# Performance work log

Hardware: AMD Instinct MI355X
Metric: run time of the kernel (lower is better)

## Reference

```python
import jax, jax.numpy as jnp
from jax import lax
import numpy as np

B = 4096          # batch
EMBED = 32        # embed_dim
HEADS = 2
MEM_SIZE = 4096
MEM_DIM = 256
TOPK = 10
LN_EPS = 1e-5


def setup_inputs() -> dict:
    key = jax.random.key(0)
    ks = jax.random.split(key, 32)
    rn = lambda i, shape, s=0.05: (jax.random.normal(ks[i], shape) * s).astype(jnp.float32)
    return {
        'x': jax.random.normal(ks[0], (B, 1, 28, 28), dtype=jnp.float32),
        'patch_w': rn(1, (32, 1, 4, 4)), 'patch_b': rn(2, (32,)),
        'blk_ln1_g': jnp.ones((2, 32), jnp.float32), 'blk_ln1_b': jnp.zeros((2, 32), jnp.float32),
        'blk_inproj_w': rn(3, (2, 96, 32)), 'blk_inproj_b': rn(4, (2, 96)),
        'blk_outproj_w': rn(5, (2, 32, 32)), 'blk_outproj_b': rn(6, (2, 32)),
        'blk_ln2_g': jnp.ones((2, 32), jnp.float32), 'blk_ln2_b': jnp.zeros((2, 32), jnp.float32),
        'blk_ff1_w': rn(7, (2, 128, 32)), 'blk_ff1_b': rn(8, (2, 128)),
        'blk_ff2_w': rn(9, (2, 32, 128)), 'blk_ff2_b': rn(10, (2, 32)),
        'lat_w': rn(11, (256, 1568)), 'lat_b': rn(12, (256,)),
        'memory': jax.random.normal(ks[13], (MEM_SIZE, MEM_DIM), dtype=jnp.float32),
        'dec_w': rn(14, (3136, 256)), 'dec_b': rn(15, (3136,)),
        'upt1_w': rn(16, (64, 32, 4, 4)), 'upt1_b': rn(17, (32,)),
        'c1_w': rn(18, (32, 32, 3, 3)), 'c1_b': rn(19, (32,)),
        'upt2_w': rn(20, (32, 16, 4, 4)), 'upt2_b': rn(21, (16,)),
        'c2_w': rn(22, (8, 16, 3, 3)), 'c2_b': rn(23, (8,)),
        'c3_w': rn(24, (1, 8, 1, 1)), 'c3_b': rn(25, (1,)),
    }


def _ln(x, g, b):
    m = jnp.mean(x, -1, keepdims=True)
    v = jnp.mean((x - m) ** 2, -1, keepdims=True)
    return (x - m) / jnp.sqrt(v + LN_EPS) * g + b


def _conv2d(x, w, b, stride=1, pad=0):
    out = lax.conv_general_dilated(x, w, (stride, stride), ((pad, pad), (pad, pad)),
                                   dimension_numbers=('NCHW', 'OIHW', 'NCHW'))
    return out + b[None, :, None, None]


def _conv_transpose2d(x, w, b, stride, pad):
    # w in torch layout [in, out, kh, kw]; equivalent fractionally-strided conv
    w_f = jnp.flip(w, (2, 3)).transpose(1, 0, 2, 3)  # OIHW
    k = w.shape[2]
    p = k - 1 - pad
    out = lax.conv_general_dilated(x, w_f, (1, 1), ((p, p), (p, p)),
                                   lhs_dilation=(stride, stride),
                                   dimension_numbers=('NCHW', 'OIHW', 'NCHW'))
    return out + b[None, :, None, None]


def _mha(x, wi, bi, wo, bo):
    Bn, S, D = x.shape
    Dh = D // HEADS
    qkv = x @ wi.T + bi                                  # [B,S,3D]
    q, k, v = jnp.split(qkv, 3, axis=-1)
    sp = lambda t: t.reshape(Bn, S, HEADS, Dh).transpose(0, 2, 1, 3)
    q, k, v = sp(q), sp(k), sp(v)
    scores = jnp.einsum('bhqd,bhkd->bhqk', q, k) / jnp.sqrt(jnp.asarray(Dh, x.dtype))
    att = jax.nn.softmax(scores, axis=-1)
    o = jnp.einsum('bhqk,bhkd->bhqd', att, v).transpose(0, 2, 1, 3).reshape(Bn, S, D)
    return o @ wo.T + bo


def _memory_read(latent, memory):
    # cosine-sim topk softmax-weighted gather (F.normalize eps=1e-12)
    mn = memory / jnp.clip(jnp.linalg.norm(memory, axis=1, keepdims=True), 1e-12)
    xn = latent / jnp.clip(jnp.linalg.norm(latent, axis=1, keepdims=True), 1e-12)
    sim = xn @ mn.T                                       # [B, MEM_SIZE]
    topk_sim, topk_idx = lax.top_k(sim, TOPK)
    w = jax.nn.softmax(topk_sim, axis=1)                  # [B, TOPK]
    sel = memory[topk_idx]                                # [B, TOPK, MEM_DIM]
    return jnp.einsum('bk,bkd->bd', w, sel)


def _forward(x, patch_w, patch_b, blk_ln1_g, blk_ln1_b, blk_inproj_w, blk_inproj_b,
             blk_outproj_w, blk_outproj_b, blk_ln2_g, blk_ln2_b, blk_ff1_w, blk_ff1_b,
             blk_ff2_w, blk_ff2_b, lat_w, lat_b, memory, dec_w, dec_b,
             upt1_w, upt1_b, c1_w, c1_b, upt2_w, upt2_b, c2_w, c2_b, c3_w, c3_b):
    Bn = x.shape[0]
    h = _conv2d(x, patch_w, patch_b, stride=4)            # [B,32,7,7]
    t = h.reshape(Bn, EMBED, 49).transpose(0, 2, 1)       # [B,49,32]
    for i in range(2):                                    # two SwinBlocks
        t = t + _mha(_ln(t, blk_ln1_g[i], blk_ln1_b[i]),
                     blk_inproj_w[i], blk_inproj_b[i], blk_outproj_w[i], blk_outproj_b[i])
        f = _ln(t, blk_ln2_g[i], blk_ln2_b[i])
        f = jax.nn.gelu(f @ blk_ff1_w[i].T + blk_ff1_b[i], approximate=False)
        t = t + (f @ blk_ff2_w[i].T + blk_ff2_b[i])
    latent = t.reshape(Bn, -1) @ lat_w.T + lat_b          # [B,256]
    mem_latent = _memory_read(latent, memory)             # [B,256]
    d = (mem_latent @ dec_w.T + dec_b).reshape(Bn, 64, 7, 7)  # dropout=eval identity
    d = jax.nn.relu(_conv_transpose2d(d, upt1_w, upt1_b, 2, 1))   # [B,32,14,14]
    d = jax.nn.relu(_conv2d(d, c1_w, c1_b, 1, 1))
    d = jax.nn.relu(_conv_transpose2d(d, upt2_w, upt2_b, 2, 1))   # [B,16,28,28]
    d = jax.nn.relu(_conv2d(d, c2_w, c2_b, 1, 1))                 # [B,8,28,28]
    return _conv2d(d, c3_w, c3_b, 1, 0)                           # [B,1,28,28]


def reference(x, patch_w, patch_b, blk_ln1_g, blk_ln1_b, blk_inproj_w, blk_inproj_b,
              blk_outproj_w, blk_outproj_b, blk_ln2_g, blk_ln2_b, blk_ff1_w, blk_ff1_b,
              blk_ff2_w, blk_ff2_b, lat_w, lat_b, memory, dec_w, dec_b,
              upt1_w, upt1_b, c1_w, c1_b, upt2_w, upt2_b, c2_w, c2_b, c3_w, c3_b):
    return _forward(x, patch_w, patch_b, blk_ln1_g, blk_ln1_b, blk_inproj_w, blk_inproj_b,
                    blk_outproj_w, blk_outproj_b, blk_ln2_g, blk_ln2_b, blk_ff1_w, blk_ff1_b,
                    blk_ff2_w, blk_ff2_b, lat_w, lat_b, memory, dec_w, dec_b,
                    upt1_w, upt1_b, c1_w, c1_b, upt2_w, upt2_b, c2_w, c2_b, c3_w, c3_b)
```

## Files before the change

### kernel.cpp

```cpp
#include <hip/hip_runtime.h>
#include <math.h>

#define B_TOT 4096
#define CHUNK 4096

typedef _Float16 half_t;
typedef _Float16 h2 __attribute__((ext_vector_type(2)));
typedef _Float16 h8v __attribute__((ext_vector_type(8)));
typedef float f4v __attribute__((ext_vector_type(4)));
typedef float f2v __attribute__((ext_vector_type(2)));

#if __has_builtin(__builtin_amdgcn_fdot2)
#define FDOT2(a, b, c) __builtin_amdgcn_fdot2((a), (b), (c), false)
#else
#define FDOT2(a, b, c) fmaf((float)(a)[1], (float)(b)[1], fmaf((float)(a)[0], (float)(b)[0], (c)))
#endif

#define KSTR 36
#define VSTR 34
#define KBYTES (49 * 72)
#define WAVE_LDS (49 * 72 + 49 * 136)
#define WI_OFF  (4 * WAVE_LDS)
#define BLOCK_LDS (WI_OFF + 12288)

__global__ __launch_bounds__(256) void k_tokens(
    const float* __restrict__ x, const float* __restrict__ pw, const float* __restrict__ pb,
    const float* __restrict__ ln1g, const float* __restrict__ ln1b,
    const float* __restrict__ wi, const float* __restrict__ bi,
    const float* __restrict__ wo, const float* __restrict__ bo,
    const float* __restrict__ ln2g, const float* __restrict__ ln2b,
    const float* __restrict__ w1, const float* __restrict__ fb1,
    const float* __restrict__ w2t, const float* __restrict__ fb2,
    float* __restrict__ tokens)
{
    __shared__ __align__(16) unsigned char Lraw[BLOCK_LDS];
    const int tid = threadIdx.x;
    const int wv = tid >> 6, lane = tid & 63;
    const int b = blockIdx.x * 4 + wv;
    half_t* Kb = (half_t*)(Lraw + wv * WAVE_LDS);
    float*  Vb = (float*)(Lraw + wv * WAVE_LDS + KBYTES);
    const float* wiL = (const float*)(Lraw + WI_OFF);
    float* Lf = (float*)Lraw;
    const bool is_tok = lane < 49;
    const int s = is_tok ? lane : 48;
    const int py = s / 7, px = s % 7;

    {
        const float4* srcw = (const float4*)(wi);
        float4* dstw = (float4*)(Lraw + WI_OFF);
        for (int e = tid; e < 768; e += 256) dstw[e] = srcw[e];
    }

    f2v xv2[8];
    const float* xb = x + (size_t)b * 784 + py * 112 + px * 4;
    #pragma unroll
    for (int r = 0; r < 4; ++r) {
        float4 vq = *(const float4*)(xb + r * 28);
        f2v lo; lo[0] = vq.x; lo[1] = vq.y;
        f2v hi; hi[0] = vq.z; hi[1] = vq.w;
        xv2[2 * r] = lo; xv2[2 * r + 1] = hi;
    }
    f2v t2[16];
    #pragma unroll
    for (int c = 0; c < 32; ++c) {
        const float* wr = pw + c * 16;
        f2v a2 = (f2v){0.f, 0.f};
        #pragma unroll
        for (int c2 = 0; c2 < 4; ++c2) {
            float4 wq = *(const float4*)&wr[4 * c2];
            f2v w0; w0[0] = wq.x; w0[1] = wq.y;
            f2v w1v; w1v[0] = wq.z; w1v[1] = wq.w;
            a2 += xv2[2 * c2] * w0;
            a2 += xv2[2 * c2 + 1] * w1v;
        }
        t2[c >> 1][c & 1] = pb[c] + a2[0] + a2[1];
    }

    for (int blk = 0; blk < 2; ++blk) {
        const float* bib = bi + blk * 96;

        f2v mu2 = (f2v){0.f, 0.f};
        #pragma unroll
        for (int i = 0; i < 16; ++i) mu2 += t2[i];
        float mu = (mu2[0] + mu2[1]) * 0.03125f;
        f2v mub; mub[0] = mu; mub[1] = mu;
        f2v var2 = (f2v){0.f, 0.f};
        #pragma unroll
        for (int i = 0; i < 16; ++i) { f2v d = t2[i] - mub; var2 += d * d; }
        float rstd = rsqrtf((var2[0] + var2[1]) * 0.03125f + 1e-5f);
        f2v rstd2; rstd2[0] = rstd; rstd2[1] = rstd;
        f2v xn2[16];
        {
            const f2v* g2 = (const f2v*)(ln1g + blk * 32);
            const f2v* bl2 = (const f2v*)(ln1b + blk * 32);
            #pragma unroll
            for (int i = 0; i < 16; ++i)
                xn2[i] = (t2[i] - mub) * rstd2 * g2[i] + bl2[i];
        }

        __syncthreads();

        #pragma unroll 4
        for (int d = 0; d < 32; ++d) {
            const float* wr = wiL + (32 + d) * 32;
            f2v a2 = (f2v){0.f, 0.f};
            #pragma unroll
            for (int c2 = 0; c2 < 8; ++c2) {
                float4 wq = *(const float4*)&wr[4 * c2];
                f2v w0; w0[0] = wq.x; w0[1] = wq.y;
                f2v w1v; w1v[0] = wq.z; w1v[1] = wq.w;
                a2 += xn2[2 * c2] * w0;
                a2 += xn2[2 * c2 + 1] * w1v;
            }
            if (is_tok) Kb[s * KSTR + d] = (half_t)(bib[32 + d] + a2[0] + a2[1]);
        }
        #pragma unroll 4
        for (int d = 0; d < 32; ++d) {
            const float* wr = wiL + (64 + d) * 32;
            f2v a2 = (f2v){0.f, 0.f};
            #pragma unroll
            for (int c2 = 0; c2 < 8; ++c2) {
                float4 wq = *(const float4*)&wr[4 * c2];
                f2v w0; w0[0] = wq.x; w0[1] = wq.y;
                f2v w1v; w1v[0] = wq.z; w1v[1] = wq.w;
                a2 += xn2[2 * c2] * w0;
                a2 += xn2[2 * c2 + 1] * w1v;
            }
            if (is_tok) Vb[s * VSTR + d] = bib[64 + d] + a2[0] + a2[1];
        }
        float q0[32];
        #pragma unroll 4
        for (int d = 0; d < 32; ++d) {
            const float* wr = wiL + d * 32;
            f2v a2 = (f2v){0.f, 0.f};
            #pragma unroll
            for (int c2 = 0; c2 < 8; ++c2) {
                float4 wq = *(const float4*)&wr[4 * c2];
                f2v w0; w0[0] = wq.x; w0[1] = wq.y;
                f2v w1v; w1v[0] = wq.z; w1v[1] = wq.w;
                a2 += xn2[2 * c2] * w0;
                a2 += xn2[2 * c2 + 1] * w1v;
            }
            q0[d] = (bib[d] + a2[0] + a2[1]) * 0.25f;
        }
        h2 qh[16];
        #pragma unroll
        for (int i = 0; i < 16; ++i) {
            h2 hh; hh[0] = (half_t)q0[2 * i]; hh[1] = (half_t)q0[2 * i + 1];
            qh[i] = hh;
        }

        __asm__ volatile("s_waitcnt lgkmcnt(0)" ::: "memory");

        f2v o2[16];
        #pragma unroll
        for (int i = 0; i < 16; ++i) o2[i] = (f2v){0.f, 0.f};
        float l0 = 0.f, l1 = 0.f;
        union H4 { double qd; h2 p[2]; };
        for (int j = 0; j < 49; ++j) {
            const double* kr = (const double*)(Kb + j * KSTR);
            const float* vr = Vb + j * VSTR;
            H4 u0, u1, u2, u3, w0, w1h, w2h, w3;
            u0.qd = kr[0]; u1.qd = kr[1]; u2.qd = kr[2]; u3.qd = kr[3];
            w0.qd = kr[4]; w1h.qd = kr[5]; w2h.qd = kr[6]; w3.qd = kr[7];
            float s0a = 0.f, s0b = 0.f, s1a = 0.f, s1b = 0.f;
            s0a = FDOT2(u0.p[0], qh[0], s0a); s0a = FDOT2(u0.p[1], qh[1], s0a);
            s0b = FDOT2(u1.p[0], qh[2], s0b); s0b = FDOT2(u1.p[1], qh[3], s0b);
            s0a = FDOT2(u2.p[0], qh[4], s0a); s0a = FDOT2(u2.p[1], qh[5], s0a);
            s0b = FDOT2(u3.p[0], qh[6], s0b); s0b = FDOT2(u3.p[1], qh[7], s0b);
            s1a = FDOT2(w0.p[0], qh[8], s1a); s1a = FDOT2(w0.p[1], qh[9], s1a);
            s1b = FDOT2(w1h.p[0], qh[10], s1b); s1b = FDOT2(w1h.p[1], qh[11], s1b);
            s1a = FDOT2(w2h.p[0], qh[12], s1a); s1a = FDOT2(w2h.p[1], qh[13], s1a);
            s1b = FDOT2(w3.p[0], qh[14], s1b); s1b = FDOT2(w3.p[1], qh[15], s1b);
            float p0 = __expf(s0a + s0b), p1 = __expf(s1a + s1b);
            l0 += p0; l1 += p1;
            f2v p02; p02[0] = p0; p02[1] = p0;
            f2v p12; p12[0] = p1; p12[1] = p1;
            #pragma unroll
            for (int i = 0; i < 8; ++i) {
                f2v va = *(const f2v*)&vr[2 * i];
                o2[i] += p02 * va;
                f2v vc = *(const f2v*)&vr[16 + 2 * i];
                o2[8 + i] += p12 * vc;
            }
        }
        {
            float il0 = 1.f / l0, il1 = 1.f / l1;
            f2v il02; il02[0] = il0; il02[1] = il0;
            f2v il12; il12[0] = il1; il12[1] = il1;
            #pragma unroll
            for (int i = 0; i < 8; ++i) { o2[i] *= il02; o2[8 + i] *= il12; }
        }

        #pragma unroll
        for (int c = 0; c < 32; ++c) {
            const float* wr = wo + blk * 1024 + c * 32;
            f2v a2 = (f2v){0.f, 0.f};
            #pragma unroll
            for (int c2 = 0; c2 < 8; ++c2) {
                float4 wq = *(const float4*)&wr[4 * c2];
                f2v w0; w0[0] = wq.x; w0[1] = wq.y;
                f2v w1v; w1v[0] = wq.z; w1v[1] = wq.w;
                a2 += o2[2 * c2] * w0;
                a2 += o2[2 * c2 + 1] * w1v;
            }
            t2[c >> 1][c & 1] += bo[blk * 32 + c] + a2[0] + a2[1];
        }

        mu2 = (f2v){0.f, 0.f};
        #pragma unroll
        for (int i = 0; i < 16; ++i) mu2 += t2[i];
        mu = (mu2[0] + mu2[1]) * 0.03125f;
        mub[0] = mu; mub[1] = mu;
        var2 = (f2v){0.f, 0.f};
        #pragma unroll
        for (int i = 0; i < 16; ++i) { f2v d = t2[i] - mub; var2 += d * d; }
        rstd = rsqrtf((var2[0] + var2[1]) * 0.03125f + 1e-5f);
        rstd2[0] = rstd; rstd2[1] = rstd;
        {
            const f2v* g2 = (const f2v*)(ln2g + blk * 32);
            const f2v* bl2 = (const f2v*)(ln2b + blk * 32);
            #pragma unroll
            for (int i = 0; i < 16; ++i)
                xn2[i] = (t2[i] - mub) * rstd2 * g2[i] + bl2[i];
        }

        __syncthreads();

        {
            const float4* src1 = (const float4*)(w1 + blk * 4096);
            const float4* src2 = (const float4*)(w2t + blk * 4096);
            float4* dst = (float4*)Lraw;
            for (int e = tid; e < 1024; e += 256) dst[e] = src1[e];
            for (int e = tid; e < 1024; e += 256) dst[1024 + e] = src2[e];
            if (blk == 0) {
                const float4* srcw = (const float4*)(wi + 3072);
                float4* dstw = (float4*)(Lraw + WI_OFF);
                for (int e = tid; e < 768; e += 256) dstw[e] = srcw[e];
            }
        }
        __syncthreads();

        const float* w2L = Lf + 4096;
        #pragma unroll 2
        for (int j = 0; j < 128; ++j) {
            const float* wr = Lf + j * 32;
            f2v h2a = (f2v){0.f, 0.f};
            #pragma unroll
            for (int c2 = 0; c2 < 8; ++c2) {
                float4 wq = *(const float4*)&wr[4 * c2];
                f2v w0; w0[0] = wq.x; w0[1] = wq.y;
                f2v w1v; w1v[0] = wq.z; w1v[1] = wq.w;
                h2a += xn2[2 * c2] * w0;
                h2a += xn2[2 * c2 + 1] * w1v;
            }
            float h = fb1[blk * 128 + j] + h2a[0] + h2a[1];
            h = 0.5f * h * (1.f + erff(h * 0.7071067811865476f));
            f2v hh; hh[0] = h; hh[1] = h;
            const float* w2r = w2L + j * 32;
            #pragma unroll
            for (int c2 = 0; c2 < 8; ++c2) {
                float4 wq = *(const float4*)&w2r[4 * c2];
                f2v w0; w0[0] = wq.x; w0[1] = wq.y;
                f2v w1v; w1v[0] = wq.z; w1v[1] = wq.w;
                t2[2 * c2]     += hh * w0;
                t2[2 * c2 + 1] += hh * w1v;
            }
        }
        {
            const f2v* fb22 = (const f2v*)(fb2 + blk * 32);
            #pragma unroll
            for (int i = 0; i < 16; ++i) t2[i] += fb22[i];
        }
    }

    if (is_tok) {
        float* op = tokens + (size_t)b * 1568 + s * 32;
        #pragma unroll
        for (int i = 0; i < 8; ++i) {
            float4 vv = make_float4(t2[2 * i][0], t2[2 * i][1],
                                    t2[2 * i + 1][0], t2[2 * i + 1][1]);
            *(float4*)&op[4 * i] = vv;
        }
    }
}

__global__ __launch_bounds__(256) void k_split(
    const float* __restrict__ lat_w, const float* __restrict__ memory,
    half_t* __restrict__ lwh, half_t* __restrict__ lwl,
    half_t* __restrict__ memh, half_t* __restrict__ meml,
    float* __restrict__ inv_norm)
{
    __shared__ float red[256];
    const int tid = threadIdx.x;
    size_t i = (size_t)blockIdx.x * 256 + tid;
    if (i < 401408) {
        float v = lat_w[i];
        half_t h = (half_t)v;
        lwh[i] = h; lwl[i] = (half_t)((v - (float)h) * 2048.0f);
    }
    float v = 0.f;
    if (i < 1048576) {
        v = memory[i];
        half_t h = (half_t)v;
        memh[i] = h; meml[i] = (half_t)((v - (float)h) * 2048.0f);
    }
    if (blockIdx.x < 4096) {
        red[tid] = v * v;
        __syncthreads();
        for (int s = 128; s > 0; s >>= 1) {
            if (tid < s) red[tid] += red[tid + s];
            __syncthreads();
        }
        if (tid == 0) inv_norm[blockIdx.x] = 1.f / fmaxf(sqrtf(red[0]), 1e-12f);
    }
}

__global__ __launch_bounds__(256) void k_sgemm(
    const float* __restrict__ A, const half_t* __restrict__ Bhg,
    const half_t* __restrict__ Blg, const float* __restrict__ bias,
    float* __restrict__ C, int M, int N, int K)
{
    __shared__ __align__(16) half_t Ah[64 * 40];
    __shared__ __align__(16) half_t Al[64 * 40];
    __shared__ __align__(16) half_t Bh[128 * 40];
    __shared__ __align__(16) half_t Bl[128 * 40];
    const int tid = threadIdx.x;
    const int n0 = blockIdx.x * 128, m0 = blockIdx.y * 64;
    const int w = tid >> 6, lane = tid & 63;
    const int wm = (w >> 1) * 32, wn = (w & 1) * 64;
    const int lr = lane & 15, lk = lane >> 4;

    const int ar = tid >> 2, aseg = (tid & 3) * 8;
    const int br = tid >> 1, bseg = (tid & 1) * 16;

    f4v acch[2][4], accm[2][4];
    #pragma unroll
    for (int i = 0; i < 2; ++i)
        #pragma unroll
        for (int j = 0; j < 4; ++j) {
            acch[i][j] = (f4v){0.f, 0.f, 0.f, 0.f};
            accm[i][j] = (f4v){0.f, 0.f, 0.f, 0.f};
        }

    for (int k0 = 0; k0 < K; k0 += 32) {
        {
            const float* ap = A + (size_t)(m0 + ar) * K + k0 + aseg;
            float4 a0 = *(const float4*)ap;
            float4 a1 = *(const float4*)(ap + 4);
            float av[8] = {a0.x, a0.y, a0.z, a0.w, a1.x, a1.y, a1.z, a1.w};
            h8v ah, al;
            #pragma unroll
            for (int i = 0; i < 8; ++i) {
                half_t h = (half_t)av[i];
                ah[i] = h;
                al[i] = (half_t)((av[i] - (float)h) * 2048.0f);
            }
            *(h8v*)&Ah[ar * 40 + aseg] = ah;
            *(h8v*)&Al[ar * 40 + aseg] = al;

            const half_t* bph = Bhg + (size_t)(n0 + br) * K + k0 + bseg;
            const half_t* bpl = Blg + (size_t)(n0 + br) * K + k0 + bseg;
            h8v bh0 = *(const h8v*)bph;
            h8v bh1 = *(const h8v*)(bph + 8);
            h8v bl0 = *(const h8v*)bpl;
            h8v bl1 = *(const h8v*)(bpl + 8);
            *(h8v*)&Bh[br * 40 + bseg]     = bh0;
            *(h8v*)&Bh[br * 40 + bseg + 8] = bh1;
            *(h8v*)&Bl[br * 40 + bseg]     = bl0;
            *(h8v*)&Bl[br * 40 + bseg + 8] = bl1;
        }
        __syncthreads();
        h8v afh[2], afl[2], bfh[4], bfl[4];
        #pragma unroll
        for (int i = 0; i < 2; ++i) {
            afh[i] = *(const h8v*)&Ah[(wm + i * 16 + lr) * 40 + lk * 8];
            afl[i] = *(const h8v*)&Al[(wm + i * 16 + lr) * 40 + lk * 8];
        }
        #pragma unroll
        for (int j = 0; j < 4; ++j) {
            bfh[j] = *(const h8v*)&Bh[(wn + j * 16 + lr) * 40 + lk * 8];
            bfl[j] = *(const h8v*)&Bl[(wn + j * 16 + lr) * 40 + lk * 8];
        }
        #pragma unroll
        for (int i = 0; i < 2; ++i)
            #pragma unroll
            for (int j = 0; j < 4; ++j) {
                acch[i][j] = __builtin_amdgcn_mfma_f32_16x16x32_f16(afh[i], bfh[j], acch[i][j], 0, 0, 0);
                accm[i][j] = __builtin_amdgcn_mfma_f32_16x16x32_f16(afh[i], bfl[j], accm[i][j], 0, 0, 0);
                accm[i][j] = __builtin_amdgcn_mfma_f32_16x16x32_f16(afl[i], bfh[j], accm[i][j], 0, 0, 0);
            }
        __syncthreads();
    }

    #pragma unroll
    for (int j = 0; j < 4; ++j) {
        int n = n0 + wn + j * 16 + lr;
        float bv = bias ? bias[n] : 0.f;
        #pragma unroll
        for (int i = 0; i < 2; ++i) {
            #pragma unroll
            for (int r = 0; r < 4; ++r) {
                int m = m0 + wm + i * 16 + lk * 4 + r;
                C[(size_t)m * N + n] = acch[i][j][r] + accm[i][j][r] * (1.0f / 2048.0f) + bv;
            }
        }
    }
}

__global__ __launch_bounds__(256) void k_dgemm(
    const float* __restrict__ A, const float* __restrict__ Bm,
    const float* __restrict__ bias, half_t* __restrict__ C,
    int M, int N, int K)
{
    __shared__ __align__(16) half_t As[64 * 40];
    __shared__ __align__(16) half_t Bs[128 * 40];
    const int tid = threadIdx.x;
    const int n0 = blockIdx.x * 128, m0 = blockIdx.y * 64;
    const int w = tid >> 6, lane = tid & 63;
    const int wm = (w >> 1) * 32, wn = (w & 1) * 64;
    const int lr = lane & 15, lk = lane >> 4;

    const int ar = tid >> 2, aseg = (tid & 3) * 8;
    const int br = tid >> 1, bseg = (tid & 1) * 16;

    f4v acc[2][4];
    #pragma unroll
    for (int i = 0; i < 2; ++i)
        #pragma unroll
        for (int j = 0; j < 4; ++j) acc[i][j] = (f4v){0.f, 0.f, 0.f, 0.f};

    for (int k0 = 0; k0 < K; k0 += 32) {
        {
            const float* ap = A + (size_t)(m0 + ar) * K + k0 + aseg;
            float4 a0 = *(const float4*)ap;
            float4 a1 = *(const float4*)(ap + 4);
            h8v ha;
            ha[0] = (half_t)a0.x; ha[1] = (half_t)a0.y;
            ha[2] = (half_t)a0.z; ha[3] = (half_t)a0.w;
            ha[4] = (half_t)a1.x; ha[5] = (half_t)a1.y;
            ha[6] = (half_t)a1.z; ha[7] = (half_t)a1.w;
            *(h8v*)&As[ar * 40 + aseg] = ha;

            const float* bp = Bm + (size_t)(n0 + br) * K + k0 + bseg;
            float4 b0 = *(const float4*)bp;
            float4 b1 = *(const float4*)(bp + 4);
            float4 b2 = *(const float4*)(bp + 8);
            float4 b3 = *(const float4*)(bp + 12);
            h8v hb0, hb1;
            hb0[0] = (half_t)b0.x; hb0[1] = (half_t)b0.y;
            hb0[2] = (half_t)b0.z; hb0[3] = (half_t)b0.w;
            hb0[4] = (half_t)b1.x; hb0[5] = (half_t)b1.y;
            hb0[6] = (half_t)b1.z; hb0[7] = (half_t)b1.w;
            hb1[0] = (half_t)b2.x; hb1[1] = (half_t)b2.y;
            hb1[2] = (half_t)b2.z; hb1[3] = (half_t)b2.w;
            hb1[4] = (half_t)b3.x; hb1[5] = (half_t)b3.y;
            hb1[6] = (half_t)b3.z; hb1[7] = (half_t)b3.w;
            *(h8v*)&Bs[br * 40 + bseg] = hb0;
            *(h8v*)&Bs[br * 40 + bseg + 8] = hb1;
        }
        __syncthreads();
        h8v af[2], bfr[4];
        #pragma unroll
        for (int i = 0; i < 2; ++i)
            af[i] = *(const h8v*)&As[(wm + i * 16 + lr) * 40 + lk * 8];
        #pragma unroll
        for (int j = 0; j < 4; ++j)
            bfr[j] = *(const h8v*)&Bs[(wn + j * 16 + lr) * 40 + lk * 8];
        #pragma unroll
        for (int i = 0; i < 2; ++i)
            #pragma unroll
            for (int j = 0; j < 4; ++j)
                acc[i][j] = __builtin_amdgcn_mfma_f32_16x16x32_f16(af[i], bfr[j], acc[i][j], 0, 0, 0);
        __syncthreads();
    }

    #pragma unroll
    for (int j = 0; j < 4; ++j) {
        int n = n0 + wn + j * 16 + lr;
        float bv = bias[n];
        #pragma unroll
        for (int i = 0; i < 2; ++i) {
            #pragma unroll
            for (int r = 0; r < 4; ++r) {
                int m = m0 + wm + i * 16 + lk * 4 + r;
                C[(size_t)m * N + n] = (half_t)fmaxf(acc[i][j][r] + bv, 0.f);
            }
        }
    }
}

__global__ __launch_bounds__(256) void k_fuse(
    const float* __restrict__ wt1, const float* __restrict__ upt1_b,
    const float* __restrict__ dec_w, const float* __restrict__ dec_b,
    float* __restrict__ Wf, float* __restrict__ bf)
{
    __shared__ float WL[4][64][32];
    const int p = blockIdx.x;
    const int k = threadIdx.x;
    const int y = p / 14, x = p % 14;

    int ky0 = 0, iy0 = 0, ky1 = 0, iy1 = 0, nky = 0;
    for (int ky = 0; ky < 4; ++ky) {
        int iyn = y + 1 - ky;
        if (iyn < 0 || (iyn & 1)) continue;
        int iy = iyn >> 1;
        if (iy > 6) continue;
        if (nky == 0) { ky0 = ky; iy0 = iy; } else { ky1 = ky; iy1 = iy; }
        ++nky;
    }
    int kx0 = 0, ix0 = 0, kx1 = 0, ix1 = 0, nkx = 0;
    for (int kx = 0; kx < 4; ++kx) {
        int ixn = x + 1 - kx;
        if (ixn < 0 || (ixn & 1)) continue;
        int ix = ixn >> 1;
        if (ix > 6) continue;
        if (nkx == 0) { kx0 = kx; ix0 = ix; } else { kx1 = kx; ix1 = ix; }
        ++nkx;
    }
    const int ntap = nky * nkx;

    for (int e = k; e < ntap * 2048; e += 256) {
        int t = e >> 11, c = (e >> 5) & 63, o = e & 31;
        int ti = (nkx == 2) ? (t >> 1) : t;
        int tj = (nkx == 2) ? (t & 1) : 0;
        int ky = ti ? ky1 : ky0;
        int kx = tj ? kx1 : kx0;
        WL[t][c][o] = wt1[((c * 32 + o) * 4 + ky) * 4 + kx];
    }
    __syncthreads();

    f2v acc2[16];
    #pragma unroll
    for (int o = 0; o < 16; ++o) acc2[o] = (f2v){0.f, 0.f};
    float bacc = 0.f;

    for (int t = 0; t < ntap; ++t) {
        int ti = (nkx == 2) ? (t >> 1) : t;
        int tj = (nkx == 2) ? (t & 1) : 0;
        int iy = ti ? iy1 : iy0;
        int ix = tj ? ix1 : ix0;
        int rbase = iy * 7 + ix;
        for (int c = 0; c < 64; ++c) {
            int row = c * 49 + rbase;
            float v = dec_w[(size_t)row * 256 + k];
            f2v vv; vv[0] = v; vv[1] = v;
            const f2v* w2p = (const f2v*)&WL[t][c][0];
            #pragma unroll
            for (int o2 = 0; o2 < 16; ++o2) acc2[o2] += vv * w2p[o2];
            if (k < 32) bacc = fmaf(WL[t][c][k], dec_b[row], bacc);
        }
    }

    #pragma unroll 4
    for (int o = 0; o < 32; ++o)
        Wf[((size_t)(p * 32 + o)) * 256 + k] = acc2[o >> 1][o & 1];
    if (k < 32) bf[p * 32 + k] = bacc + upt1_b[k];
}

__global__ __launch_bounds__(256) void k_memread(
    const float* __restrict__ latent, const float* __restrict__ dots,
    const float* __restrict__ inv_mn, const float* __restrict__ mem,
    float* __restrict__ out)
{
    __shared__ float red[256];
    __shared__ int   redi[4];
    __shared__ float inv_x_s;
    const int b = blockIdx.x, tid = threadIdx.x;
    const int w = tid >> 6, lane = tid & 63;
    float lx = latent[(size_t)b * 256 + tid];
    red[tid] = lx * lx;
    __syncthreads();
    for (int s = 128; s > 0; s >>= 1) {
        if (tid < s) red[tid] += red[tid + s];
        __syncthreads();
    }
    if (tid == 0) inv_x_s = 1.f / fmaxf(sqrtf(red[0]), 1e-12f);
    __syncthreads();
    const float inv_x = inv_x_s;

    float vals[16];
    for (int j = 0; j < 16; ++j) {
        int m = tid + j * 256;
        vals[j] = dots[(size_t)b * 4096 + m] * inv_mn[m] * inv_x;
    }
    float tv[10]; int ti[10];
    for (int t = 0; t < 10; ++t) {
        float bv = -1e30f; int bidx = 0x7fffffff;
        #pragma unroll
        for (int j = 0; j < 16; ++j) {
            int m = tid + j * 256;
            float v = vals[j];
            if (v > bv || (v == bv && m < bidx)) { bv = v; bidx = m; }
        }
        #pragma unroll
        for (int off = 32; off > 0; off >>= 1) {
            float ov = __shfl_xor(bv, off);
            int   oi = __shfl_xor(bidx, off);
            if (ov > bv || (ov == bv && oi < bidx)) { bv = ov; bidx = oi; }
        }
        if (lane == 0) { red[w] = bv; redi[w] = bidx; }
        __syncthreads();
        float fv = red[0]; int fi = redi[0];
        #pragma unroll
        for (int q = 1; q < 4; ++q) {
            float v2 = red[q]; int i2 = redi[q];
            if (v2 > fv || (v2 == fv && i2 < fi)) { fv = v2; fi = i2; }
        }
        tv[t] = fv; ti[t] = fi;
        if ((fi & 255) == tid) vals[fi >> 8] = -1e30f;
        __syncthreads();
    }
    float wgt[10], wsum = 0.f;
    for (int t = 0; t < 10; ++t) { wgt[t] = expf(tv[t] - tv[0]); wsum += wgt[t]; }
    float inv_ws = 1.f / wsum;
    float acc = 0.f;
    for (int t = 0; t < 10; ++t) acc += (wgt[t] * inv_ws) * mem[(size_t)ti[t] * 256 + tid];
    out[(size_t)b * 256 + tid] = acc;
}

__global__ __launch_bounds__(256) void k_pack(
    const float* __restrict__ wc1, const float* __restrict__ wt2,
    const float* __restrict__ wc2, const float* __restrict__ w2src,
    half_t* __restrict__ pk2h, half_t* __restrict__ pk3h,
    float* __restrict__ pk4, float* __restrict__ pk5)
{
    int i = blockIdx.x * 256 + threadIdx.x;
    if (i < 9216) {
        int ic = i & 31, oc = (i >> 5) & 15, nt = (i >> 9) & 1, t = i >> 10;
        pk2h[i] = (half_t)wc1[((nt * 16 + oc) * 32 + ic) * 9 + t];
    }
    if (i < 8192) {
        int ic = i & 31, oc = (i >> 5) & 15, t = (i >> 9) & 3, q = i >> 11;
        int wy = t >> 1, wx = t & 1, py = q >> 1, px = q & 1;
        int ky = 3 - py - 2 * wy, kx = 3 - px - 2 * wx;
        pk3h[i] = (half_t)wt2[((ic * 16 + oc) * 4 + ky) * 4 + kx];
    }
    if (i < 1152) {
        int o = i & 7, tap = (i >> 3) % 9, c = i / 72;
        pk4[i] = wc2[(o * 16 + c) * 9 + tap];
    }
    if (i < 8192) {
        int c = i & 31, j = (i >> 5) & 127, bq = i >> 12;
        pk5[i] = w2src[bq * 4096 + c * 128 + j];
    }
}

__global__ __launch_bounds__(256) void k_conv1(
    const half_t* __restrict__ in, const half_t* __restrict__ wh,
    const float* __restrict__ bias, half_t* __restrict__ out)
{
    __shared__ __align__(16) half_t P[2 * 16 * 16 * 40];
    const int tid = threadIdx.x;
    const int w = tid >> 6, lane = tid & 63;
    const size_t b0 = (size_t)blockIdx.x * 2;

    for (int e = tid; e < 10240; e += 256) ((unsigned int*)P)[e] = 0u;
    __syncthreads();
    {
        const unsigned int* src = (const unsigned int*)in;
        for (int e = tid; e < 6272; e += 256) {
            int si = e / 3136;
            int rem = e - si * 3136;
            int p = rem >> 4, c2 = rem & 15;
            int y = p / 14, x = p % 14;
            ((unsigned int*)P)[si * 5120 + ((y + 1) * 16 + (x + 1)) * 20 + c2] =
                src[(b0 + si) * 3136 + rem];
        }
    }

    h8v bfr[9][2];
    #pragma unroll
    for (int t = 0; t < 9; ++t)
        #pragma unroll
        for (int nt = 0; nt < 2; ++nt)
            bfr[t][nt] = *(const h8v*)&wh[((size_t)((t * 2 + nt) * 16 + (lane & 15))) * 32 + (lane >> 4) * 8];

    __syncthreads();

    const int kseg = (lane >> 4) * 8;
    const int oc = lane & 15;
    const float bv0 = bias[oc], bv1 = bias[16 + oc];

    for (int job = w; job < 26; job += 4) {
        const int si = job >= 13 ? 1 : 0;
        const int tile = job - si * 13;
        int p = tile * 16 + (lane & 15);
        if (p > 195) p = 195;
        const int y = p / 14, x = p % 14;
        const half_t* Pb = P + si * 10240;

        f4v acc0 = (f4v){0.f, 0.f, 0.f, 0.f};
        f4v acc1 = (f4v){0.f, 0.f, 0.f, 0.f};
        #pragma unroll
        for (int ky = 0; ky < 3; ++ky) {
            #pragma unroll
            for (int kx = 0; kx < 3; ++kx) {
                h8v af = *(const h8v*)&Pb[((y + ky) * 16 + (x + kx)) * 40 + kseg];
                acc0 = __builtin_amdgcn_mfma_f32_16x16x32_f16(af, bfr[ky * 3 + kx][0], acc0, 0, 0, 0);
                acc1 = __builtin_amdgcn_mfma_f32_16x16x32_f16(af, bfr[ky * 3 + kx][1], acc1, 0, 0, 0);
            }
        }

        const int pr0 = tile * 16 + (lane >> 4) * 4;
        half_t* ob = out + (b0 + si) * 6272;
        #pragma unroll
        for (int r = 0; r < 4; ++r) {
            int pp = pr0 + r;
            if (pp < 196) {
                ob[(size_t)pp * 32 + oc]      = (half_t)fmaxf(acc0[r] + bv0, 0.f);
                ob[(size_t)pp * 32 + 16 + oc] = (half_t)fmaxf(acc1[r] + bv1, 0.f);
            }
        }
    }
}

__global__ __launch_bounds__(256) void k_convt23(
    const half_t* __restrict__ in, const half_t* __restrict__ pk3h,
    const float* __restrict__ bt2, const float* __restrict__ pk4,
    const float* __restrict__ b2, const float* __restrict__ w3,
    const float* __restrict__ b3, float* __restrict__ out)
{
    __shared__ __align__(16) unsigned char Lraw[30720];
    half_t* Pin = (half_t*)Lraw;
    float*  P2  = (float*)Lraw;
    const int tid = threadIdx.x;
    const int w = tid >> 6, lane = tid & 63;
    const int b = blockIdx.x;

    for (int e = tid; e < 5120; e += 256) ((unsigned int*)Pin)[e] = 0u;
    __syncthreads();
    {
        const unsigned int* src = (const unsigned int*)in;
        for (int e = tid; e < 3136; e += 256) {
            int p = e >> 4, c2 = e & 15;
            int y = p / 14, x = p % 14;
            ((unsigned int*)Pin)[((y + 1) * 16 + (x + 1)) * 20 + c2] =
                src[(size_t)b * 3136 + e];
        }
    }
    __syncthreads();

    const int oc = lane & 15;
    const int kseg = (lane >> 4) * 8;

    f4v res[13];
    #pragma unroll
    for (int j = 0; j < 13; ++j) {
        const int job = w + 4 * j;
        const int q = job / 13, tile = job - q * 13;
        const int py = q >> 1, px = q & 1;
        int p = tile * 16 + (lane & 15);
        if (p > 195) p = 195;
        const int ty = p / 14, tx = p % 14;
        f4v a = (f4v){0.f, 0.f, 0.f, 0.f};
        #pragma unroll
        for (int t = 0; t < 4; ++t) {
            const int wy = t >> 1, wx = t & 1;
            h8v bf = *(const h8v*)&pk3h[((size_t)((q * 4 + t) * 16 + oc)) * 32 + kseg];
            h8v af = *(const h8v*)&Pin[((ty + py + wy) * 16 + (tx + px + wx)) * 40 + kseg];
            a = __builtin_amdgcn_mfma_f32_16x16x32_f16(af, bf, a, 0, 0, 0);
        }
        res[j] = a;
    }
    __syncthreads();

    const bool active2 = tid < 196;
    int row = active2 ? tid / 7 : 0;
    int tx0b = active2 ? (tid % 7) * 4 : 0;
    const float bco = bt2[oc];

    f2v acc2[4][4];
    #pragma unroll
    for (int i = 0; i < 4; ++i)
        #pragma unroll
        for (int o2 = 0; o2 < 4; ++o2) acc2[i][o2] = (f2v){0.f, 0.f};

    #pragma unroll
    for (int g = 0; g < 2; ++g) {
        for (int e = tid; e < 7680; e += 256) P2[e] = 0.f;
        __syncthreads();
        if ((oc >> 3) == g) {
            #pragma unroll
            for (int j = 0; j < 13; ++j) {
                const int job = w + 4 * j;
                const int q = job / 13, tile = job - q * 13;
                const int py = q >> 1, px = q & 1;
                const int pr0 = tile * 16 + (lane >> 4) * 4;
                #pragma unroll
                for (int r = 0; r < 4; ++r) {
                    int p = pr0 + r;
                    if (p < 196) {
                        int Y = 2 * (p / 14) + py, X = 2 * (p % 14) + px;
                        P2[((oc & 7) * 30 + Y + 1) * 32 + (X + 1)] = fmaxf(res[j][r] + bco, 0.f);
                    }
                }
            }
        }
        __syncthreads();
        for (int cl = 0; cl < 8; ++cl) {
            const float* Pb = &P2[(cl * 30 + row) * 32 + tx0b];
            const float* wb = pk4 + (size_t)(g * 8 + cl) * 72;
            #pragma unroll
            for (int ky = 0; ky < 3; ++ky) {
                float4 a = *(const float4*)&Pb[ky * 32];
                float4 bq = *(const float4*)&Pb[ky * 32 + 4];
                float rowb[8] = {a.x, a.y, a.z, a.w, bq.x, bq.y, bq.z, bq.w};
                #pragma unroll
                for (int kx = 0; kx < 3; ++kx) {
                    const f2v* wt2p = (const f2v*)(wb + (ky * 3 + kx) * 8);
                    #pragma unroll
                    for (int i = 0; i < 4; ++i) {
                        f2v rb; rb[0] = rowb[i + kx]; rb[1] = rowb[i + kx];
                        acc2[i][0] += rb * wt2p[0];
                        acc2[i][1] += rb * wt2p[1];
                        acc2[i][2] += rb * wt2p[2];
                        acc2[i][3] += rb * wt2p[3];
                    }
                }
            }
        }
        __syncthreads();
    }

    if (active2) {
        const float bias3 = b3[0];
        #pragma unroll
        for (int i = 0; i < 4; ++i) {
            float r = bias3;
            #pragma unroll
            for (int o = 0; o < 8; ++o)
                r += fmaxf(acc2[i][o >> 1][o & 1] + b2[o], 0.f) * w3[o];
            out[(size_t)b * 784 + row * 28 + tx0b + i] = r;
        }
    }
}

extern "C" void kernel_launch(void* const* d_in, const int* in_sizes, int n_in,
                              void* d_out, int out_size, void* d_ws, size_t ws_size,
                              hipStream_t stream)
{
    const float* x       = (const float*)d_in[0];
    const float* patch_w = (const float*)d_in[1];
    const float* patch_b = (const float*)d_in[2];
    const float* ln1g    = (const float*)d_in[3];
    const float* ln1b    = (const float*)d_in[4];
    const float* wi      = (const float*)d_in[5];
    const float* bi      = (const float*)d_in[6];
    const float* wo      = (const float*)d_in[7];
    const float* bo      = (const float*)d_in[8];
    const float* ln2g    = (const float*)d_in[9];
    const float* ln2b    = (const float*)d_in[10];
    const float* w1      = (const float*)d_in[11];
    const float* b1      = (const float*)d_in[12];
    const float* w2      = (const float*)d_in[13];
    const float* b2      = (const float*)d_in[14];
    const float* lat_w   = (const float*)d_in[15];
    const float* lat_b   = (const float*)d_in[16];
    const float* memory  = (const float*)d_in[17];
    const float* dec_w   = (const float*)d_in[18];
    const float* dec_b   = (const float*)d_in[19];
    const float* upt1_w  = (const float*)d_in[20];
    const float* upt1_b  = (const float*)d_in[21];
    const float* c1_w    = (const float*)d_in[22];
    const float* c1_b    = (const float*)d_in[23];
    const float* upt2_w  = (const float*)d_in[24];
    const float* upt2_b  = (const float*)d_in[25];
    const float* c2_w    = (const float*)d_in[26];
    const float* c2_b    = (const float*)d_in[27];
    const float* c3_w    = (const float*)d_in[28];
    const float* c3_b    = (const float*)d_in[29];
    float* outp = (float*)d_out;

    float* ws = (float*)d_ws;
    size_t off = 0;
    auto alloc = [&](size_t n) { float* p = ws + off; off += (n + 63) & ~(size_t)63; return p; };
    float* tokens     = alloc((size_t)B_TOT * 1568);
    float* latent     = alloc((size_t)B_TOT * 256);
    float* dots       = alloc((size_t)B_TOT * 4096);
    float* mem_latent = alloc((size_t)B_TOT * 256);
    float* inv_mn     = alloc(4096);
    half_t* pk2h      = (half_t*)alloc(4608);
    half_t* pk3h      = (half_t*)alloc(4096);
    float* pk4        = alloc(1152);
    float* pk5        = alloc(8192);
    float* Wf         = alloc((size_t)6272 * 256);
    float* bf         = alloc(6272);
    half_t* d1h       = (half_t*)alloc((size_t)CHUNK * 6272 / 2);
    half_t* d2h       = (half_t*)alloc((size_t)CHUNK * 6272 / 2);
    half_t* lwh       = (half_t*)alloc(200704);
    half_t* lwl       = (half_t*)alloc(200704);
    half_t* memh      = (half_t*)alloc(524288);
    half_t* meml      = (half_t*)alloc(524288);
    (void)in_sizes; (void)n_in; (void)out_size; (void)ws_size;

    k_pack<<<36, 256, 0, stream>>>(c1_w, upt2_w, c2_w, w2, pk2h, pk3h, pk4, pk5);
    k_split<<<4096, 256, 0, stream>>>(lat_w, memory, lwh, lwl, memh, meml, inv_mn);
    k_fuse<<<196, 256, 0, stream>>>(upt1_w, upt1_b, dec_w, dec_b, Wf, bf);

    k_tokens<<<B_TOT / 4, 256, 0, stream>>>(x, patch_w, patch_b, ln1g, ln1b, wi, bi,
                                            wo, bo, ln2g, ln2b, w1, b1, pk5, b2, tokens);
    k_sgemm<<<dim3(256 / 128, B_TOT / 64), 256, 0, stream>>>(tokens, lwh, lwl, lat_b,
                                                             latent, B_TOT, 256, 1568);
    k_sgemm<<<dim3(4096 / 128, B_TOT / 64), 256, 0, stream>>>(latent, memh, meml, nullptr,
                                                              dots, B_TOT, 4096, 256);
    k_memread<<<B_TOT, 256, 0, stream>>>(latent, dots, inv_mn, memory, mem_latent);

    for (int c = 0; c < B_TOT / CHUNK; ++c) {
        const float* ml = mem_latent + (size_t)c * CHUNK * 256;
        k_dgemm<<<dim3(6272 / 128, CHUNK / 64), 256, 0, stream>>>(ml, Wf, bf, d1h,
                                                                  CHUNK, 6272, 256);
        k_conv1  <<<CHUNK / 2, 256, 0, stream>>>(d1h, pk2h, c1_b, d2h);
        k_convt23<<<CHUNK, 256, 0, stream>>>(d2h, pk3h, upt2_b, pk4, c2_b, c3_w, c3_b,
                                             outp + (size_t)c * CHUNK * 784);
    }
}
```

Baseline: 1.042 ms.

## Fuse conv1 into the convtranspose/conv2/conv3 kernel via shared memory

Merges the 3x3 conv1 kernel into the following transposed-conv/conv2/conv3 kernel, so each block computes conv1 for one sample and writes the padded result into a second LDS buffer instead of to global memory. This removes the d2h intermediate buffer's global write and read and one kernel launch. In exchange, LDS per block grows from 30 KB to 40 KB and more registers are held for the conv1 weights, which may lower occupancy. Each block now handles one sample for conv1 rather than two.

```diff
diff --git a/kernel.cpp b/kernel.cpp
--- a/kernel.cpp
+++ b/kernel.cpp
@@ -646,103 +646,76 @@
     }
 }
 
-__global__ __launch_bounds__(256) void k_conv1(
+__global__ __launch_bounds__(256) void k_c123(
     const half_t* __restrict__ in, const half_t* __restrict__ wh,
-    const float* __restrict__ bias, half_t* __restrict__ out)
-{
-    __shared__ __align__(16) half_t P[2 * 16 * 16 * 40];
-    const int tid = threadIdx.x;
-    const int w = tid >> 6, lane = tid & 63;
-    const size_t b0 = (size_t)blockIdx.x * 2;
-
-    for (int e = tid; e < 10240; e += 256) ((unsigned int*)P)[e] = 0u;
-    __syncthreads();
-    {
-        const unsigned int* src = (const unsigned int*)in;
-        for (int e = tid; e < 6272; e += 256) {
-            int si = e / 3136;
-            int rem = e - si * 3136;
-            int p = rem >> 4, c2 = rem & 15;
-            int y = p / 14, x = p % 14;
-            ((unsigned int*)P)[si * 5120 + ((y + 1) * 16 + (x + 1)) * 20 + c2] =
-                src[(b0 + si) * 3136 + rem];
-        }
-    }
-
-    h8v bfr[9][2];
-    #pragma unroll
-    for (int t = 0; t < 9; ++t)
-        #pragma unroll
-        for (int nt = 0; nt < 2; ++nt)
-            bfr[t][nt] = *(const h8v*)&wh[((size_t)((t * 2 + nt) * 16 + (lane & 15))) * 32 + (lane >> 4) * 8];
-
-    __syncthreads();
-
-    const int kseg = (lane >> 4) * 8;
-    const int oc = lane & 15;
-    const float bv0 = bias[oc], bv1 = bias[16 + oc];
-
-    for (int job = w; job < 26; job += 4) {
-        const int si = job >= 13 ? 1 : 0;
-        const int tile = job - si * 13;
-        int p = tile * 16 + (lane & 15);
-        if (p > 195) p = 195;
-        const int y = p / 14, x = p % 14;
-        const half_t* Pb = P + si * 10240;
-
-        f4v acc0 = (f4v){0.f, 0.f, 0.f, 0.f};
-        f4v acc1 = (f4v){0.f, 0.f, 0.f, 0.f};
-        #pragma unroll
-        for (int ky = 0; ky < 3; ++ky) {
-            #pragma unroll
-            for (int kx = 0; kx < 3; ++kx) {
-                h8v af = *(const h8v*)&Pb[((y + ky) * 16 + (x + kx)) * 40 + kseg];
-                acc0 = __builtin_amdgcn_mfma_f32_16x16x32_f16(af, bfr[ky * 3 + kx][0], acc0, 0, 0, 0);
-                acc1 = __builtin_amdgcn_mfma_f32_16x16x32_f16(af, bfr[ky * 3 + kx][1], acc1, 0, 0, 0);
-            }
-        }
-
-        const int pr0 = tile * 16 + (lane >> 4) * 4;
-        half_t* ob = out + (b0 + si) * 6272;
-        #pragma unroll
-        for (int r = 0; r < 4; ++r) {
-            int pp = pr0 + r;
-            if (pp < 196) {
-                ob[(size_t)pp * 32 + oc]      = (half_t)fmaxf(acc0[r] + bv0, 0.f);
-                ob[(size_t)pp * 32 + 16 + oc] = (half_t)fmaxf(acc1[r] + bv1, 0.f);
-            }
-        }
-    }
-}
-
-__global__ __launch_bounds__(256) void k_convt23(
-    const half_t* __restrict__ in, const half_t* __restrict__ pk3h,
+    const float* __restrict__ b1c, const half_t* __restrict__ pk3h,
     const float* __restrict__ bt2, const float* __restrict__ pk4,
     const float* __restrict__ b2, const float* __restrict__ w3,
     const float* __restrict__ b3, float* __restrict__ out)
 {
-    __shared__ __align__(16) unsigned char Lraw[30720];
-    half_t* Pin = (half_t*)Lraw;
-    float*  P2  = (float*)Lraw;
+    __shared__ __align__(16) unsigned char Lraw[40960];
+    half_t* A  = (half_t*)Lraw;
+    half_t* Bt = (half_t*)(Lraw + 20480);
+    float*  P2 = (float*)Lraw;
     const int tid = threadIdx.x;
     const int w = tid >> 6, lane = tid & 63;
     const int b = blockIdx.x;
 
-    for (int e = tid; e < 5120; e += 256) ((unsigned int*)Pin)[e] = 0u;
+    for (int e = tid; e < 10240; e += 256) ((unsigned int*)Lraw)[e] = 0u;
     __syncthreads();
     {
         const unsigned int* src = (const unsigned int*)in;
         for (int e = tid; e < 3136; e += 256) {
             int p = e >> 4, c2 = e & 15;
             int y = p / 14, x = p % 14;
-            ((unsigned int*)Pin)[((y + 1) * 16 + (x + 1)) * 20 + c2] =
+            ((unsigned int*)A)[((y + 1) * 16 + (x + 1)) * 20 + c2] =
                 src[(size_t)b * 3136 + e];
         }
     }
-    __syncthreads();
 
     const int oc = lane & 15;
     const int kseg = (lane >> 4) * 8;
+
+    h8v bfr1[9][2];
+    #pragma unroll
+    for (int t = 0; t < 9; ++t)
+        #pragma unroll
+        for (int nt = 0; nt < 2; ++nt)
+            bfr1[t][nt] = *(const h8v*)&wh[((size_t)((t * 2 + nt) * 16 + oc)) * 32 + kseg];
+
+    __syncthreads();
+
+    {
+        const float bv0 = b1c[oc], bv1 = b1c[16 + oc];
+        for (int tile = w; tile < 13; tile += 4) {
+            int p = tile * 16 + (lane & 15);
+            if (p > 195) p = 195;
+            const int y = p / 14, x = p % 14;
+            f4v acc0 = (f4v){0.f, 0.f, 0.f, 0.f};
+            f4v acc1 = (f4v){0.f, 0.f, 0.f, 0.f};
+            #pragma unroll
+            for (int ky = 0; ky < 3; ++ky) {
+                #pragma unroll
+                for (int kx = 0; kx < 3; ++kx) {
+                    h8v af = *(const h8v*)&A[((y + ky) * 16 + (x + kx)) * 40 + kseg];
+                    acc0 = __builtin_amdgcn_mfma_f32_16x16x32_f16(af, bfr1[ky * 3 + kx][0], acc0, 0, 0, 0);
+                    acc1 = __builtin_amdgcn_mfma_f32_16x16x32_f16(af, bfr1[ky * 3 + kx][1], acc1, 0, 0, 0);
+                }
+            }
+            const int pr0 = tile * 16 + (lane >> 4) * 4;
+            #pragma unroll
+            for (int r = 0; r < 4; ++r) {
+                int pp = pr0 + r;
+                if (pp < 196) {
+                    int yy = pp / 14, xx = pp % 14;
+                    int base = ((yy + 1) * 16 + (xx + 1)) * 40;
+                    Bt[base + oc]      = (half_t)fmaxf(acc0[r] + bv0, 0.f);
+                    Bt[base + 16 + oc] = (half_t)fmaxf(acc1[r] + bv1, 0.f);
+                }
+            }
+        }
+    }
+    __syncthreads();
 
     f4v res[13];
     #pragma unroll
@@ -758,7 +731,7 @@
         for (int t = 0; t < 4; ++t) {
             const int wy = t >> 1, wx = t & 1;
             h8v bf = *(const h8v*)&pk3h[((size_t)((q * 4 + t) * 16 + oc)) * 32 + kseg];
-            h8v af = *(const h8v*)&Pin[((ty + py + wy) * 16 + (tx + px + wx)) * 40 + kseg];
+            h8v af = *(const h8v*)&Bt[((ty + py + wy) * 16 + (tx + px + wx)) * 40 + kseg];
             a = __builtin_amdgcn_mfma_f32_16x16x32_f16(af, bf, a, 0, 0, 0);
         }
         res[j] = a;
@@ -887,7 +860,6 @@
     float* Wf         = alloc((size_t)6272 * 256);
     float* bf         = alloc(6272);
     half_t* d1h       = (half_t*)alloc((size_t)CHUNK * 6272 / 2);
-    half_t* d2h       = (half_t*)alloc((size_t)CHUNK * 6272 / 2);
     half_t* lwh       = (half_t*)alloc(200704);
     half_t* lwl       = (half_t*)alloc(200704);
     half_t* memh      = (half_t*)alloc(524288);
@@ -910,8 +882,8 @@
         const float* ml = mem_latent + (size_t)c * CHUNK * 256;
         k_dgemm<<<dim3(6272 / 128, CHUNK / 64), 256, 0, stream>>>(ml, Wf, bf, d1h,
                                                                   CHUNK, 6272, 256);
-        k_conv1  <<<CHUNK / 2, 256, 0, stream>>>(d1h, pk2h, c1_b, d2h);
-        k_convt23<<<CHUNK, 256, 0, stream>>>(d2h, pk3h, upt2_b, pk4, c2_b, c3_w, c3_b,
-                                             outp + (size_t)c * CHUNK * 784);
+        k_c123<<<CHUNK, 256, 0, stream>>>(d1h, pk2h, c1_b, pk3h, upt2_b, pk4,
+                                          c2_b, c3_w, c3_b,
+                                          outp + (size_t)c * CHUNK * 784);
     }
 }
```

New measurement: 1.015 ms. -2.6%, faster.
